# Performance work log

Measured on AMD Instinct MI355X. Metric: run time of the kernel, lower is better.

The kernel has to match this reference:

```python
import jax, jax.numpy as jnp
import numpy as np

BATCH = 2048
NUM_FIELDS = 32
EMBED = 64
NPAIRS = NUM_FIELDS * (NUM_FIELDS - 1) // 2  # 496
# static pair indices (i < j), same order as the torch double loop
ROW, COL = np.triu_indices(NUM_FIELDS, k=1)
ROW = jnp.asarray(ROW)
COL = jnp.asarray(COL)


def setup_inputs() -> dict:
    key = jax.random.key(0)
    k1, k2 = jax.random.split(key)
    emb_inputs = jax.random.normal(k1, (BATCH, NUM_FIELDS, EMBED), dtype=jnp.float32)
    # xavier_normal_ on kernel of shape (E, NC2, E): fan_in = NC2*E (dims[1:]), fan_out = E*E... 
    # torch: fan_in = size(1)*receptive = NPAIRS*EMBED? torch uses size(1)*prod(size[2:]) = NPAIRS*EMBED,
    # fan_out = size(0)*prod(size[2:]) = EMBED*EMBED; std = sqrt(2/(fan_in+fan_out))
    fan_in = NPAIRS * EMBED
    fan_out = EMBED * EMBED
    std = float(np.sqrt(2.0 / (fan_in + fan_out)))
    kernel = jax.random.normal(k2, (EMBED, NPAIRS, EMBED), dtype=jnp.float32) * std
    return {"emb_inputs": emb_inputs, "kernel": kernel}


def reference(emb_inputs, kernel):
    # emb_inputs: (B, N, E); kernel: (E, NC2, E)
    p = emb_inputs[:, ROW]  # (B, NC2, E)
    q = emb_inputs[:, COL]  # (B, NC2, E)
    # torch: kp[b,i,pair] = sum_j p[b,pair,j] * kernel[i,pair,j]; out[b,pair] = sum_i kp*q
    kp = jnp.einsum('bpj,ipj->bpi', p, kernel)  # (B, NC2, E) -- avoids (B,E,NC2,E) blowup
    outputs = jnp.sum(kp * q, axis=-1)          # (B, NC2)
    return outputs[:, None, :]                  # (B, 1, NC2)
```

## Files before the change

kernel.cpp:

```cpp
#include <hip/hip_runtime.h>
#include <hip/hip_bf16.h>
#include <math.h>

#define BATCH   2048
#define NFIELDS 32
#define EMBED   64
#define NPAIRS  496

typedef __attribute__((ext_vector_type(8))) short bf16x8;
typedef __attribute__((ext_vector_type(4))) float f32x4;

__device__ __forceinline__ unsigned short f2bf(float x) {
    unsigned int u = __float_as_uint(x);
    unsigned int r = 0x7fffu + ((u >> 16) & 1u);
    return (unsigned short)((u + r) >> 16);
}
__device__ __forceinline__ float bf2f(unsigned short b) {
    return __uint_as_float(((unsigned int)b) << 16);
}
__device__ __forceinline__ bf16x8 cvt8(const float* p) {
    float4 v0 = *(const float4*)p;
    float4 v1 = *(const float4*)(p + 4);
    bf16x8 o;
    o[0]=(short)f2bf(v0.x); o[1]=(short)f2bf(v0.y); o[2]=(short)f2bf(v0.z); o[3]=(short)f2bf(v0.w);
    o[4]=(short)f2bf(v1.x); o[5]=(short)f2bf(v1.y); o[6]=(short)f2bf(v1.z); o[7]=(short)f2bf(v1.w);
    return o;
}

__global__ __launch_bounds__(256) void convert_prepass(
    const float* __restrict__ emb, const float* __restrict__ kern,
    unsigned short* __restrict__ embB, unsigned short* __restrict__ kernB)
{
    const int EMB4 = BATCH * NFIELDS * EMBED / 4;
    const int KER4 = EMBED * NPAIRS * EMBED / 4;
    int t = blockIdx.x * blockDim.x + threadIdx.x;
    if (t < EMB4) {
        float4 v = ((const float4*)emb)[t];
        ushort4 o;
        o.x = f2bf(v.x); o.y = f2bf(v.y); o.z = f2bf(v.z); o.w = f2bf(v.w);
        *(ushort4*)(embB + (size_t)t * 4) = o;
    } else if (t < EMB4 + KER4) {
        int u = t - EMB4;
        int j4   = u & 15;
        int rest = u >> 4;
        int p = rest % NPAIRS;
        int i = rest / NPAIRS;
        float4 v = *(const float4*)(kern + (size_t)i * (NPAIRS*EMBED) + (size_t)p * EMBED + j4*4);
        ushort4 o;
        o.x = f2bf(v.x); o.y = f2bf(v.y); o.z = f2bf(v.z); o.w = f2bf(v.w);
        *(ushort4*)(kernB + (size_t)p * 4096 + i * 64 + j4 * 4) = o;
    }
}

template<bool PRE>
__global__ __launch_bounds__(256, 4) void opn_fused(
    const void* __restrict__ embP, const void* __restrict__ kernP,
    const float* __restrict__ embF, float* __restrict__ out)
{
    const int bid   = blockIdx.x;
    const int chunk = bid >> 3;
    const int bt    = bid & 7;

    const int tid  = threadIdx.x;
    const int wave = tid >> 6, lane = tid & 63;
    const int col  = lane & 15, quad = lane >> 4;
    const int pair = chunk * 4 + wave;

    int r;
    {
        float sq = sqrtf((float)(3969 - 8 * pair));
        r = (int)((63.0f - sq) * 0.5f);
        if (r > 0 && r * (63 - r) / 2 > pair) --r;
        if ((r + 1) * (63 - (r + 1)) / 2 <= pair) ++r;
    }
    const int c = r + 1 + (pair - r * (63 - r) / 2);

    __shared__ __align__(16) float Otile[256][4];

    bf16x8 kfr[4][2];
    if (PRE) {
        const unsigned short* kb = (const unsigned short*)kernP + (size_t)pair * 4096;
        #pragma unroll
        for (int nt = 0; nt < 4; ++nt)
            #pragma unroll
            for (int ks = 0; ks < 2; ++ks)
                kfr[nt][ks] = *(const bf16x8*)(kb + (nt*16 + col) * 64 + ks*32 + quad*8);
    } else {
        const float* kf = (const float*)kernP;
        #pragma unroll
        for (int nt = 0; nt < 4; ++nt)
            #pragma unroll
            for (int ks = 0; ks < 2; ++ks)
                kfr[nt][ks] = cvt8(kf + (size_t)(nt*16 + col) * (NPAIRS*EMBED)
                                     + (size_t)pair * EMBED + ks*32 + quad*8);
    }

    float res[16];

    #pragma unroll
    for (int it = 0; it < 16; ++it) {
        const int brow = bt * 256 + it * 16 + col;

        bf16x8 bfr0, bfr1;
        ushort4 qv[4];
        if (PRE) {
            const unsigned short* eb = (const unsigned short*)embP
                                     + ((size_t)brow * NFIELDS + r) * EMBED;
            bfr0 = *(const bf16x8*)(eb + quad*8);
            bfr1 = *(const bf16x8*)(eb + 32 + quad*8);
            const unsigned short* qb = (const unsigned short*)embP
                                     + ((size_t)brow * NFIELDS + c) * EMBED + quad*4;
            #pragma unroll
            for (int nt = 0; nt < 4; ++nt)
                qv[nt] = *(const ushort4*)(qb + nt*16);
        } else {
            const float* ef = (const float*)embP + ((size_t)brow * NFIELDS + r) * EMBED;
            bfr0 = cvt8(ef + quad*8);
            bfr1 = cvt8(ef + 32 + quad*8);
            const float* qp = embF + ((size_t)brow * NFIELDS + c) * EMBED + quad*4;
            #pragma unroll
            for (int nt = 0; nt < 4; ++nt) {
                f32x4 q = *(const f32x4*)(qp + nt*16);
                qv[nt].x = f2bf(q[0]); qv[nt].y = f2bf(q[1]);
                qv[nt].z = f2bf(q[2]); qv[nt].w = f2bf(q[3]);
            }
        }

        float partial = 0.f;
        #pragma unroll
        for (int nt = 0; nt < 4; ++nt) {
            f32x4 acc = {0.f, 0.f, 0.f, 0.f};
            acc = __builtin_amdgcn_mfma_f32_16x16x32_bf16(kfr[nt][0], bfr0, acc, 0, 0, 0);
            acc = __builtin_amdgcn_mfma_f32_16x16x32_bf16(kfr[nt][1], bfr1, acc, 0, 0, 0);
            partial += acc[0]*bf2f(qv[nt].x) + acc[1]*bf2f(qv[nt].y)
                     + acc[2]*bf2f(qv[nt].z) + acc[3]*bf2f(qv[nt].w);
        }
        partial += __shfl_xor(partial, 16, 64);
        partial += __shfl_xor(partial, 32, 64);
        res[it] = partial;
    }

    if (quad == 0) {
        #pragma unroll
        for (int it = 0; it < 16; ++it)
            Otile[it*16 + col][wave] = res[it];
    }
    __syncthreads();

    {
        f32x4 o = *(const f32x4*)&Otile[tid][0];
        *(f32x4*)&out[((size_t)(bt*256 + tid)) * NPAIRS + chunk*4] = o;
    }
}

extern "C" void kernel_launch(void* const* d_in, const int* in_sizes, int n_in,
                              void* d_out, int out_size, void* d_ws, size_t ws_size,
                              hipStream_t stream) {
    const float* emb  = (const float*)d_in[0];
    const float* kern = (const float*)d_in[1];
    float* out = (float*)d_out;

    const size_t embElems  = (size_t)BATCH * NFIELDS * EMBED;
    const size_t kernElems = (size_t)EMBED * NPAIRS * EMBED;
    const size_t need = (embElems + kernElems) * sizeof(unsigned short);

    if (ws_size >= need) {
        unsigned short* embB  = (unsigned short*)d_ws;
        unsigned short* kernB = embB + embElems;
        int total4 = (int)((embElems + kernElems) / 4);
        convert_prepass<<<(total4 + 255) / 256, 256, 0, stream>>>(emb, kern, embB, kernB);
        opn_fused<true><<<dim3(992), 256, 0, stream>>>(
            (const void*)embB, (const void*)kernB, emb, out);
    } else {
        opn_fused<false><<<dim3(992), 256, 0, stream>>>(
            (const void*)emb, (const void*)kern, emb, out);
    }
}
```

Before: 120.7 us.

## Double-buffer embedding rows into LDS via async global_load_lds

After: 107.9 us. 1.12x faster.

```diff
diff --git a/kernel.cpp b/kernel.cpp
--- a/kernel.cpp
+++ b/kernel.cpp
@@ -75,6 +75,7 @@
     }
     const int c = r + 1 + (pair - r * (63 - r) / 2);
 
+    __shared__ __align__(16) unsigned short Stage[4][2][2][1024];
     __shared__ __align__(16) float Otile[256][4];
 
     bf16x8 kfr[4][2];
@@ -97,47 +98,97 @@
 
     float res[16];
 
-    #pragma unroll
-    for (int it = 0; it < 16; ++it) {
-        const int brow = bt * 256 + it * 16 + col;
-
-        bf16x8 bfr0, bfr1;
-        ushort4 qv[4];
-        if (PRE) {
-            const unsigned short* eb = (const unsigned short*)embP
-                                     + ((size_t)brow * NFIELDS + r) * EMBED;
-            bfr0 = *(const bf16x8*)(eb + quad*8);
-            bfr1 = *(const bf16x8*)(eb + 32 + quad*8);
-            const unsigned short* qb = (const unsigned short*)embP
-                                     + ((size_t)brow * NFIELDS + c) * EMBED + quad*4;
+    if (PRE) {
+        const unsigned short* eb = (const unsigned short*)embP;
+        const int rr = lane & 15;
+        const int ss = lane >> 4;
+        const int brow0 = bt * 256;
+        const unsigned short* gr = eb + ((size_t)(brow0 + rr) * NFIELDS + r) * EMBED + ss*8;
+        const unsigned short* gc = eb + ((size_t)(brow0 + rr) * NFIELDS + c) * EMBED + ss*8;
+        const size_t itstride = (size_t)16 * NFIELDS * EMBED;
+
+        const unsigned offB0 = (unsigned)quad * 256 + (unsigned)col * 16;
+        const unsigned offB1 = offB0 + 1024;
+        unsigned offQ[4];
+        #pragma unroll
+        for (int nt = 0; nt < 4; ++nt)
+            offQ[nt] = (unsigned)(2*nt + (quad >> 1)) * 256
+                     + (unsigned)col * 16 + (unsigned)(quad & 1) * 8;
+
+        #define STAGE(itv, bufv) do {                                                     \
+            const unsigned short* _r = gr + (size_t)(itv) * itstride;                     \
+            const unsigned short* _c = gc + (size_t)(itv) * itstride;                     \
+            __builtin_amdgcn_global_load_lds(                                             \
+                (const __attribute__((address_space(1))) void*)_r,                        \
+                (__attribute__((address_space(3))) void*)&Stage[wave][bufv][0][0],   16, 0, 0); \
+            __builtin_amdgcn_global_load_lds(                                             \
+                (const __attribute__((address_space(1))) void*)(_r + 32),                 \
+                (__attribute__((address_space(3))) void*)&Stage[wave][bufv][0][512], 16, 0, 0); \
+            __builtin_amdgcn_global_load_lds(                                             \
+                (const __attribute__((address_space(1))) void*)_c,                        \
+                (__attribute__((address_space(3))) void*)&Stage[wave][bufv][1][0],   16, 0, 0); \
+            __builtin_amdgcn_global_load_lds(                                             \
+                (const __attribute__((address_space(1))) void*)(_c + 32),                 \
+                (__attribute__((address_space(3))) void*)&Stage[wave][bufv][1][512], 16, 0, 0); \
+        } while (0)
+
+        STAGE(0, 0);
+
+        #pragma unroll
+        for (int it = 0; it < 16; ++it) {
+            const int buf = it & 1;
+            if (it < 15) {
+                STAGE(it + 1, buf ^ 1);
+                asm volatile("s_waitcnt vmcnt(4)" ::: "memory");
+            } else {
+                asm volatile("s_waitcnt vmcnt(0)" ::: "memory");
+            }
+            __builtin_amdgcn_sched_barrier(0);
+
+            const char* rb = (const char*)&Stage[wave][buf][0][0];
+            const char* cb = (const char*)&Stage[wave][buf][1][0];
+            bf16x8 bfr0 = *(const bf16x8*)(rb + offB0);
+            bf16x8 bfr1 = *(const bf16x8*)(rb + offB1);
+            ushort4 qv[4];
             #pragma unroll
             for (int nt = 0; nt < 4; ++nt)
-                qv[nt] = *(const ushort4*)(qb + nt*16);
-        } else {
+                qv[nt] = *(const ushort4*)(cb + offQ[nt]);
+
+            float partial = 0.f;
+            #pragma unroll
+            for (int nt = 0; nt < 4; ++nt) {
+                f32x4 acc = {0.f, 0.f, 0.f, 0.f};
+                acc = __builtin_amdgcn_mfma_f32_16x16x32_bf16(kfr[nt][0], bfr0, acc, 0, 0, 0);
+                acc = __builtin_amdgcn_mfma_f32_16x16x32_bf16(kfr[nt][1], bfr1, acc, 0, 0, 0);
+                partial += acc[0]*bf2f(qv[nt].x) + acc[1]*bf2f(qv[nt].y)
+                         + acc[2]*bf2f(qv[nt].z) + acc[3]*bf2f(qv[nt].w);
+            }
+            partial += __shfl_xor(partial, 16, 64);
+            partial += __shfl_xor(partial, 32, 64);
+            res[it] = partial;
+        }
+        #undef STAGE
+    } else {
+        #pragma unroll
+        for (int it = 0; it < 16; ++it) {
+            const int brow = bt * 256 + it * 16 + col;
             const float* ef = (const float*)embP + ((size_t)brow * NFIELDS + r) * EMBED;
-            bfr0 = cvt8(ef + quad*8);
-            bfr1 = cvt8(ef + 32 + quad*8);
+            bf16x8 bfr0 = cvt8(ef + quad*8);
+            bf16x8 bfr1 = cvt8(ef + 32 + quad*8);
             const float* qp = embF + ((size_t)brow * NFIELDS + c) * EMBED + quad*4;
+            float partial = 0.f;
             #pragma unroll
             for (int nt = 0; nt < 4; ++nt) {
                 f32x4 q = *(const f32x4*)(qp + nt*16);
-                qv[nt].x = f2bf(q[0]); qv[nt].y = f2bf(q[1]);
-                qv[nt].z = f2bf(q[2]); qv[nt].w = f2bf(q[3]);
+                f32x4 acc = {0.f, 0.f, 0.f, 0.f};
+                acc = __builtin_amdgcn_mfma_f32_16x16x32_bf16(kfr[nt][0], bfr0, acc, 0, 0, 0);
+                acc = __builtin_amdgcn_mfma_f32_16x16x32_bf16(kfr[nt][1], bfr1, acc, 0, 0, 0);
+                partial += acc[0]*q[0] + acc[1]*q[1] + acc[2]*q[2] + acc[3]*q[3];
             }
+            partial += __shfl_xor(partial, 16, 64);
+            partial += __shfl_xor(partial, 32, 64);
+            res[it] = partial;
         }
-
-        float partial = 0.f;
-        #pragma unroll
-        for (int nt = 0; nt < 4; ++nt) {
-            f32x4 acc = {0.f, 0.f, 0.f, 0.f};
-            acc = __builtin_amdgcn_mfma_f32_16x16x32_bf16(kfr[nt][0], bfr0, acc, 0, 0, 0);
-            acc = __builtin_amdgcn_mfma_f32_16x16x32_bf16(kfr[nt][1], bfr1, acc, 0, 0, 0);
-            partial += acc[0]*bf2f(qv[nt].x) + acc[1]*bf2f(qv[nt].y)
-                     + acc[2]*bf2f(qv[nt].z) + acc[3]*bf2f(qv[nt].w);
-        }
-        partial += __shfl_xor(partial, 16, 64);
-        partial += __shfl_xor(partial, 32, 64);
-        res[it] = partial;
     }
 
     if (quad == 0) {
```
